# Optimization experiments

Measured on AMD Instinct MI355X. Metric: run time of the kernel, lower is better.

The kernel has to match this reference:

```python
import jax, jax.numpy as jnp
import numpy as np

B, C, H, W = 16, 256, 32, 32
NH, DH = 16, 16          # n_heads, n_head_channels; NH*DH == C
STRIDE, KK = 2, 9        # offset conv stride / kernel (stage_idx=0)
Hk, Wk = 16, 16          # offset map size = H/stride
NS = Hk * Wk             # n_sample
EPS_LN, EPS_BN = 1e-5, 1e-5


def conv1x1(x, w, b=None):
    # x: [B,Ci,H,W], w: [Co,Ci]
    y = jnp.einsum('bihw,oi->bohw', x, w)
    if b is not None:
        y = y + b[None, :, None, None]
    return y


def dwconv(x, w, b):
    # depthwise conv, w: [C,1,KK,KK]
    y = jax.lax.conv_general_dilated(
        x, w, (STRIDE, STRIDE), [(KK // 2, KK // 2)] * 2,
        dimension_numbers=('NCHW', 'OIHW', 'NCHW'),
        feature_group_count=x.shape[1])
    return y + b[None, :, None, None]


def ln_channels(x, g, b):
    # LayerNormProxy: layer-norm over channel dim of NCHW
    m = jnp.mean(x, axis=1, keepdims=True)
    v = jnp.mean((x - m) ** 2, axis=1, keepdims=True)
    return (x - m) / jnp.sqrt(v + EPS_LN) * g[None, :, None, None] + b[None, :, None, None]


def ref_points(hk, wk, b):
    # normalized (y, x) reference grid in [-1, 1], matching _get_ref_points
    ry = (jnp.arange(hk, dtype=jnp.float32) + 0.5) / hk * 2.0 - 1.0
    rx = (jnp.arange(wk, dtype=jnp.float32) + 0.5) / wk * 2.0 - 1.0
    ref = jnp.stack(jnp.meshgrid(ry, rx, indexing='ij'), axis=-1)  # [hk,wk,2] (y,x)
    return jnp.broadcast_to(ref[None], (b, hk, wk, 2))


def grid_sample_bilinear(img, grid):
    # img: [B,C,H,W]; grid: [B,Hg,Wg,2] in (x,y) order, [-1,1], align_corners=True,
    # zeros padding (matches torch F.grid_sample defaults).
    Bi, Ci, Hi, Wi = img.shape
    gx = (grid[..., 0] + 1.0) * 0.5 * (Wi - 1)
    gy = (grid[..., 1] + 1.0) * 0.5 * (Hi - 1)
    x0 = jnp.floor(gx); y0 = jnp.floor(gy)
    x1 = x0 + 1.0;      y1 = y0 + 1.0
    wx1 = gx - x0; wx0 = 1.0 - wx1
    wy1 = gy - y0; wy0 = 1.0 - wy1
    imgf = img.reshape(Bi, Ci, Hi * Wi)

    def gather(yi, xi):
        valid = (yi >= 0) & (yi < Hi) & (xi >= 0) & (xi < Wi)
        idx = (jnp.clip(yi, 0, Hi - 1) * Wi + jnp.clip(xi, 0, Wi - 1)).astype(jnp.int32)
        v = jnp.take_along_axis(imgf, idx.reshape(Bi, 1, -1), axis=2)  # [B,C,Hg*Wg]
        return v * valid.reshape(Bi, 1, -1).astype(img.dtype)

    out = (gather(y0, x0) * (wy0 * wx0).reshape(Bi, 1, -1)
           + gather(y0, x1) * (wy0 * wx1).reshape(Bi, 1, -1)
           + gather(y1, x0) * (wy1 * wx0).reshape(Bi, 1, -1)
           + gather(y1, x1) * (wy1 * wx1).reshape(Bi, 1, -1))
    return out.reshape(Bi, Ci, grid.shape[1], grid.shape[2])


def setup_inputs() -> dict:
    key = jax.random.key(0)
    ks = jax.random.split(key, 16)
    s = 0.05
    return {
        'x':        jax.random.normal(ks[0], (B, C, H, W), jnp.float32),
        'wq':       jax.random.normal(ks[1], (C, C), jnp.float32) * s,
        'bq':       jax.random.normal(ks[2], (C,), jnp.float32) * s,
        'off_dw_w': jax.random.normal(ks[3], (C, 1, KK, KK), jnp.float32) * s,
        'off_dw_b': jax.random.normal(ks[4], (C,), jnp.float32) * s,
        'ln_g':     jnp.ones((C,), jnp.float32),
        'ln_b':     jnp.zeros((C,), jnp.float32),
        'off_pw_w': jax.random.normal(ks[5], (2, C), jnp.float32) * s,
        'wk':       jax.random.normal(ks[6], (C, C), jnp.float32) * s,
        'bk':       jax.random.normal(ks[7], (C,), jnp.float32) * s,
        'wv':       jax.random.normal(ks[8], (C, C), jnp.float32) * s,
        'bv':       jax.random.normal(ks[9], (C,), jnp.float32) * s,
        'wo':       jax.random.normal(ks[10], (C, C), jnp.float32) * s,
        'bo':       jax.random.normal(ks[11], (C,), jnp.float32) * s,
        'bn_g':     jnp.ones((C,), jnp.float32),
        'bn_b':     jnp.zeros((C,), jnp.float32),
        'bn_m':     jax.random.normal(ks[12], (C,), jnp.float32) * s,
        'bn_v':     jax.random.uniform(ks[13], (C,), jnp.float32) + 0.5,
    }


def reference(x, wq, bq, off_dw_w, off_dw_b, ln_g, ln_b, off_pw_w,
              wk, bk, wv, bv, wo, bo, bn_g, bn_b, bn_m, bn_v):
    q = conv1x1(x, wq, bq)                                 # [B,C,H,W]
    # offset branch (n_groups=1 so q_off == q)
    off = dwconv(q, off_dw_w, off_dw_b)                    # [B,C,Hk,Wk]
    off = jax.nn.gelu(ln_channels(off, ln_g, ln_b), approximate=False)
    offset = jnp.einsum('bihw,oi->bohw', off, off_pw_w)    # [B,2,Hk,Wk] (y,x)
    offset = jnp.transpose(offset, (0, 2, 3, 1))           # [B,Hk,Wk,2]
    ref = ref_points(Hk, Wk, B)
    pos = jnp.tanh(offset + ref)                           # offset_range_factor[0] < 0 branch
    # deformable sampling: grid takes (x,y)
    xs = grid_sample_bilinear(x, pos[..., ::-1])           # [B,C,Hk,Wk]
    xs = xs.reshape(B, C, 1, NS)
    k = conv1x1(xs, wk, bk).reshape(B * NH, DH, NS)
    v = conv1x1(xs, wv, bv).reshape(B * NH, DH, NS)
    qf = q.reshape(B * NH, DH, H * W)
    attn = jnp.einsum('bcm,bcn->bmn', qf, k) * (DH ** -0.5)  # [B*NH, H*W, NS]
    attn = jax.nn.softmax(attn, axis=2)
    out = jnp.einsum('bmn,bcn->bcm', attn, v).reshape(B, C, H, W)
    y = conv1x1(out, wo, bo)
    # BatchNorm2d in eval mode with running stats
    y = ((y - bn_m[None, :, None, None]) / jnp.sqrt(bn_v[None, :, None, None] + EPS_BN)
         * bn_g[None, :, None, None] + bn_b[None, :, None, None])
    return y
```

## Files before the change

kernel.cpp:

```cpp
#include <hip/hip_runtime.h>
#include <hip/hip_bf16.h>
#include <math.h>

#define BATCH 16
#define CH    256
#define HW    1024
#define NS    256
#define NH    16
#define DH    16

typedef __attribute__((ext_vector_type(8))) short short8v;
typedef __attribute__((ext_vector_type(4))) float float4v;

__device__ __forceinline__ unsigned short f2bf(float f) {
    return __builtin_bit_cast(unsigned short, __float2bfloat16(f));
}
__device__ __forceinline__ unsigned pack2(float lo, float hi) {
    return (unsigned)f2bf(lo) | ((unsigned)f2bf(hi) << 16);
}

__global__ __launch_bounds__(256) void prep_k(
    const float* __restrict__ wq, const float* __restrict__ wk,
    const float* __restrict__ wv, const float* __restrict__ wo,
    unsigned short* __restrict__ Wf,
    const float* __restrict__ x, unsigned short* __restrict__ xT)
{
    int blk = blockIdx.x;
    if (blk < 1024) {
        const float* W;
        switch (blk >> 8) {
            case 0: W = wq; break;
            case 1: W = wk; break;
            case 2: W = wv; break;
            default: W = wo; break;
        }
        int e = (blk & 255) * 256 + threadIdx.x;
        int i = e & 7, l = (e >> 3) & 63, kt = (e >> 9) & 7, ot = e >> 12;
        float v = W[(ot * 16 + (l & 15)) * 256 + kt * 32 + 8 * (l >> 4) + i];
        Wf[(blk >> 8) * 65536 + e] = f2bf(v);
    } else {
        int xb = blk - 1024;
        int b = xb >> 4, pblk = (xb >> 2) & 3, cblk = xb & 3;
        int p = pblk * 256 + threadIdx.x;
        const float* xp = x + (size_t)b * CH * HW + p;
        unsigned short* o = xT + ((size_t)b * HW + p) * CH;
        #pragma unroll
        for (int cc = 0; cc < 64; cc += 8) {
            int c0 = cblk * 64 + cc;
            short8v t;
            #pragma unroll
            for (int i = 0; i < 8; ++i) t[i] = (short)f2bf(xp[(size_t)(c0 + i) * HW]);
            *(short8v*)&o[c0] = t;
        }
    }
}

template<int P, int MODE>
__global__ __launch_bounds__(256) void gemm_k(
    const unsigned short* __restrict__ Wf, const unsigned short* __restrict__ XT,
    const float* __restrict__ bias,
    float* __restrict__ outF, unsigned short* __restrict__ outB,
    const float* __restrict__ bn_g, const float* __restrict__ bn_b,
    const float* __restrict__ bn_m, const float* __restrict__ bn_v)
{
    const int b = blockIdx.z;

    const int t = threadIdx.x, lane = t & 63, wvi = t >> 6;
    const int g = lane >> 4, col = lane & 15;
    const int o0 = blockIdx.x * 64;
    const int p0 = blockIdx.y * 128 + wvi * 32;
    const unsigned short* xb = XT + ((size_t)b * P + p0) * CH;

    float4v acc[4][2];
    #pragma unroll
    for (int mi = 0; mi < 4; ++mi)
        #pragma unroll
        for (int ni = 0; ni < 2; ++ni) {
            float4v z = {0.f, 0.f, 0.f, 0.f};
            acc[mi][ni] = z;
        }

    #pragma unroll
    for (int kt = 0; kt < 8; ++kt) {
        short8v af[4], bf[2];
        #pragma unroll
        for (int mi = 0; mi < 4; ++mi)
            af[mi] = *(const short8v*)&Wf[(((((o0 >> 4) + mi) * 8) + kt) * 64 + lane) * 8];
        #pragma unroll
        for (int ni = 0; ni < 2; ++ni) {
            if (MODE == 2) {
                const int hh = kt * 2 + (g >> 1);
                const int p  = p0 + ni * 16 + col;
                bf[ni] = *(const short8v*)&XT[(((size_t)(b * 16 + hh) * P + p) << 4) + 8 * (g & 1)];
            } else {
                bf[ni] = *(const short8v*)&xb[(size_t)(ni * 16 + col) * CH + kt * 32 + 8 * g];
            }
        }
        #pragma unroll
        for (int mi = 0; mi < 4; ++mi)
            #pragma unroll
            for (int ni = 0; ni < 2; ++ni)
                acc[mi][ni] = __builtin_amdgcn_mfma_f32_16x16x32_bf16(
                    af[mi], bf[ni], acc[mi][ni], 0, 0, 0);
    }

    #pragma unroll
    for (int mi = 0; mi < 4; ++mi) {
        const int ob = o0 + mi * 16 + 4 * g;
        float bs[4];
        #pragma unroll
        for (int ii = 0; ii < 4; ++ii) bs[ii] = bias[ob + ii];

        if (MODE == 2) {
            float sc[4], sh[4];
            #pragma unroll
            for (int ii = 0; ii < 4; ++ii) {
                int o = ob + ii;
                float s = bn_g[o] * rsqrtf(bn_v[o] + 1e-5f);
                sc[ii] = s;
                sh[ii] = bn_b[o] - bn_m[o] * s + bs[ii] * s;
            }
            #pragma unroll
            for (int ni = 0; ni < 2; ++ni) {
                int p = p0 + ni * 16 + col;
                #pragma unroll
                for (int ii = 0; ii < 4; ++ii)
                    outF[((size_t)(b * CH + ob + ii)) * P + p] =
                        acc[mi][ni][ii] * sc[ii] + sh[ii];
            }
        } else {
            const int hh = (o0 >> 4) + mi;
            #pragma unroll
            for (int ni = 0; ni < 2; ++ni) {
                int p = p0 + ni * 16 + col;
                float v0 = acc[mi][ni][0] + bs[0];
                float v1 = acc[mi][ni][1] + bs[1];
                float v2 = acc[mi][ni][2] + bs[2];
                float v3 = acc[mi][ni][3] + bs[3];
                outF[((size_t)(b * CH + ob + 0)) * P + p] = v0;
                outF[((size_t)(b * CH + ob + 1)) * P + p] = v1;
                outF[((size_t)(b * CH + ob + 2)) * P + p] = v2;
                outF[((size_t)(b * CH + ob + 3)) * P + p] = v3;
                uint2 w;
                w.x = pack2(v0 * 0.25f, v1 * 0.25f);
                w.y = pack2(v2 * 0.25f, v3 * 0.25f);
                *(uint2*)&outB[(((size_t)(b * 16 + hh) * P + p) << 4) + 4 * g] = w;
            }
        }
    }
}

__global__ __launch_bounds__(256) void dwconv_k(
    const float* __restrict__ q, const float* __restrict__ w,
    const float* __restrict__ bias, float* __restrict__ off)
{
    int bc = blockIdx.x;
    int c  = bc & (CH - 1);
    __shared__ float plane[HW];
    __shared__ float kw[81];
    int t = threadIdx.x;
    const float* qp = q + (size_t)bc * HW;
    #pragma unroll
    for (int j = t; j < HW; j += 256) plane[j] = qp[j];
    if (t < 81) kw[t] = w[c * 81 + t];
    __syncthreads();
    int hk = t >> 4, wk = t & 15;
    float s = bias[c];
    int yb = hk * 2 - 4, xb = wk * 2 - 4;
    #pragma unroll
    for (int dy = 0; dy < 9; ++dy) {
        int yy = yb + dy;
        if ((unsigned)yy < 32u) {
            #pragma unroll
            for (int dx = 0; dx < 9; ++dx) {
                int xx = xb + dx;
                if ((unsigned)xx < 32u) s += kw[dy * 9 + dx] * plane[yy * 32 + xx];
            }
        }
    }
    off[(size_t)bc * NS + t] = s;
}

__device__ inline void block_reduce2(float& a, float& b, int t, float* sbuf)
{
    #pragma unroll
    for (int o = 32; o > 0; o >>= 1) {
        a += __shfl_down(a, o);
        b += __shfl_down(b, o);
    }
    int w = t >> 6;
    if ((t & 63) == 0) { sbuf[w * 2] = a; sbuf[w * 2 + 1] = b; }
    __syncthreads();
    a = sbuf[0] + sbuf[2] + sbuf[4] + sbuf[6];
    b = sbuf[1] + sbuf[3] + sbuf[5] + sbuf[7];
    __syncthreads();
}

__global__ __launch_bounds__(256) void lngs_k(
    const float* __restrict__ off, const float* __restrict__ ln_g,
    const float* __restrict__ ln_b, const float* __restrict__ pw,
    const float* __restrict__ x, unsigned short* __restrict__ xsT)
{
    __shared__ float sbuf[8];
    int bs = blockIdx.x;
    int b = bs >> 8, s = bs & 255;
    int c = threadIdx.x;
    float v = off[((size_t)(b * CH + c)) * NS + s];
    float a = v, q2 = v * v;
    block_reduce2(a, q2, c, sbuf);
    float mean = a * (1.0f / 256.0f);
    float var  = q2 * (1.0f / 256.0f) - mean * mean;
    float xn = (v - mean) * rsqrtf(var + 1e-5f) * ln_g[c] + ln_b[c];
    float g = 0.5f * xn * (1.0f + erff(xn * 0.70710678118654752f));
    float d0 = g * pw[c];
    float d1 = g * pw[CH + c];
    block_reduce2(d0, d1, c, sbuf);

    int hk = s >> 4, wk = s & 15;
    float ry = ((hk + 0.5f) / 16.0f) * 2.0f - 1.0f;
    float rx = ((wk + 0.5f) / 16.0f) * 2.0f - 1.0f;
    float py = tanhf(d0 + ry);
    float px = tanhf(d1 + rx);

    float gx = (px + 1.0f) * 0.5f * 31.0f;
    float gy = (py + 1.0f) * 0.5f * 31.0f;
    float x0f = floorf(gx), y0f = floorf(gy);
    int ix = (int)x0f, iy = (int)y0f;
    float wx1 = gx - x0f, wx0 = 1.0f - wx1;
    float wy1 = gy - y0f, wy0 = 1.0f - wy1;
    const float* img = x + ((size_t)b * CH + c) * HW;
    float v00 = ((unsigned)iy < 32u && (unsigned)ix < 32u) ? img[iy * 32 + ix] : 0.0f;
    float v01 = ((unsigned)iy < 32u && (unsigned)(ix + 1) < 32u) ? img[iy * 32 + ix + 1] : 0.0f;
    float v10 = ((unsigned)(iy + 1) < 32u && (unsigned)ix < 32u) ? img[(iy + 1) * 32 + ix] : 0.0f;
    float v11 = ((unsigned)(iy + 1) < 32u && (unsigned)(ix + 1) < 32u) ? img[(iy + 1) * 32 + ix + 1] : 0.0f;
    float vv = wy0 * wx0 * v00 + wy0 * wx1 * v01 + wy1 * wx0 * v10 + wy1 * wx1 * v11;
    xsT[(size_t)bs * CH + c] = f2bf(vv);
}

__global__ __launch_bounds__(1024) void attn_fused_k(
    const unsigned short* __restrict__ qH, const unsigned short* __restrict__ xsT,
    const unsigned short* __restrict__ Wf,
    const float* __restrict__ bk, const float* __restrict__ bv,
    unsigned short* __restrict__ aoH)
{
    const int bh    = blockIdx.x >> 1;
    const int mhalf = blockIdx.x & 1;
    const int b = bh >> 4, h = bh & 15;

    __shared__ short Kp[16 * 32 * 8 + 8];
    __shared__ short Vp[8 * 64 * 8];
    __shared__ short Ps[16][16 * 32];

    const int tid  = threadIdx.x;
    const int lane = tid & 63;
    const int wvi  = tid >> 6;
    const int col  = lane & 15;
    const int g    = lane >> 4;

    {
        const unsigned short* WfK = Wf + 1 * 65536 + h * 4096;
        const unsigned short* WfV = Wf + 2 * 65536 + h * 4096;
        float bk4[4];
        #pragma unroll
        for (int j = 0; j < 4; ++j) bk4[j] = bk[h * 16 + 4 * g + j];
        const float bvv = bv[h * 16 + col];

        const int t  = wvi;
        const int n0 = t * 16;
        float4v accK = {0.f, 0.f, 0.f, 0.f};
        float4v accV = {0.f, 0.f, 0.f, 0.f};
        #pragma unroll
        for (int kt = 0; kt < 8; ++kt) {
            short8v xsf = *(const short8v*)&xsT[((size_t)(b * NS + n0 + col)) * CH + kt * 32 + 8 * g];
            short8v wkf = *(const short8v*)&WfK[(kt * 64 + lane) * 8];
            short8v wvf = *(const short8v*)&WfV[(kt * 64 + lane) * 8];
            accK = __builtin_amdgcn_mfma_f32_16x16x32_bf16(wkf, xsf, accK, 0, 0, 0);
            accV = __builtin_amdgcn_mfma_f32_16x16x32_bf16(xsf, wvf, accV, 0, 0, 0);
        }
        uint2 wrk;
        wrk.x = pack2(accK[0] + bk4[0], accK[1] + bk4[1]);
        wrk.y = pack2(accK[2] + bk4[2], accK[3] + bk4[3]);
        *(uint2*)&Kp[(t * 32 + (g >> 1) * 16 + col) * 8 + 4 * (g & 1)] = wrk;
        uint2 wrv;
        wrv.x = pack2(accV[0] + bvv, accV[1] + bvv);
        wrv.y = pack2(accV[2] + bvv, accV[3] + bvv);
        *(uint2*)&Vp[((t >> 1) * 64 + col + 16 * ((2 * t + (g >> 1)) & 3)) * 8 + 4 * (g & 1)] = wrv;
    }
    if (tid == 0) {
        short8v z = {0, 0, 0, 0, 0, 0, 0, 0};
        *(short8v*)&Kp[16 * 32 * 8] = z;
    }
    __syncthreads();

    const unsigned short* Qb = qH + ((size_t)(b * 16 + h) * HW << 4);
    unsigned short*       Ob = aoH + ((size_t)(b * 16 + h) * HW << 4);
    char* pbase = (char*)Ps[wvi];
    const char* kbase = (const char*)Kp + ((lane < 32) ? lane * 16 : 16 * 32 * 16);
    const int   kstep = (lane < 32) ? 512 : 0;

    #pragma unroll
    for (int mt = 0; mt < 2; ++mt) {
        const int m0 = mhalf * 512 + wvi * 32 + mt * 16;

        short8v qf = {0, 0, 0, 0, 0, 0, 0, 0};
        if (g < 2)
            qf = *(const short8v*)&Qb[((m0 + col) << 4) + 8 * g];

        float4v p[16];
        #pragma unroll
        for (int t = 0; t < 16; ++t) {
            short8v kf = *(const short8v*)(kbase + t * kstep);
            float4v z = {0.f, 0.f, 0.f, 0.f};
            p[t] = __builtin_amdgcn_mfma_f32_16x16x32_bf16(kf, qf, z, 0, 0, 0);
        }

        float mx4[16];
        #pragma unroll
        for (int t = 0; t < 16; ++t)
            mx4[t] = fmaxf(fmaxf(p[t][0], p[t][1]), fmaxf(p[t][2], p[t][3]));
        #pragma unroll
        for (int o = 8; o >= 1; o >>= 1)
            #pragma unroll
            for (int i = 0; i < 8; ++i)
                if (i < o) mx4[i] = fmaxf(mx4[i], mx4[i + o]);
        float mx = mx4[0];
        mx = fmaxf(mx, __shfl_xor(mx, 16));
        mx = fmaxf(mx, __shfl_xor(mx, 32));

        float s4[4] = {0.f, 0.f, 0.f, 0.f};
        #pragma unroll
        for (int t = 0; t < 16; ++t) {
            #pragma unroll
            for (int i = 0; i < 4; ++i) {
                float e = __expf(p[t][i] - mx);
                p[t][i] = e;
                s4[i] += e;
            }
        }
        float sum = (s4[0] + s4[1]) + (s4[2] + s4[3]);
        sum += __shfl_xor(sum, 16);
        sum += __shfl_xor(sum, 32);
        const float inv = 1.0f / sum;

        float4v acc = {0.f, 0.f, 0.f, 0.f};
        #pragma unroll
        for (int c = 0; c < 8; ++c) {
            #pragma unroll
            for (int pp = 0; pp < 2; ++pp) {
                float4v pv = p[2 * c + pp];
                uint2 wr;
                wr.x = pack2(pv[0], pv[1]);
                wr.y = pack2(pv[2], pv[3]);
                *(uint2*)(pbase + ((col * 64 + (16 * pp + 4 * g) * 2) ^ ((col & 7) << 4))) = wr;
            }
            short8v pf = *(const short8v*)(pbase + ((col * 64 + 16 * g) ^ ((col & 7) << 4)));
            short8v vf = *(const short8v*)&Vp[(c * 64 + lane) * 8];
            acc = __builtin_amdgcn_mfma_f32_16x16x32_bf16(vf, pf, acc, 0, 0, 0);
        }

        uint2 w;
        w.x = pack2(acc[0] * inv, acc[1] * inv);
        w.y = pack2(acc[2] * inv, acc[3] * inv);
        *(uint2*)&Ob[((m0 + col) << 4) + 4 * g] = w;
    }
}

extern "C" void kernel_launch(void* const* d_in, const int* in_sizes, int n_in,
                              void* d_out, int out_size, void* d_ws, size_t ws_size,
                              hipStream_t stream)
{
    const float* x        = (const float*)d_in[0];
    const float* wq       = (const float*)d_in[1];
    const float* bq       = (const float*)d_in[2];
    const float* off_dw_w = (const float*)d_in[3];
    const float* off_dw_b = (const float*)d_in[4];
    const float* ln_g     = (const float*)d_in[5];
    const float* ln_b     = (const float*)d_in[6];
    const float* off_pw_w = (const float*)d_in[7];
    const float* wk       = (const float*)d_in[8];
    const float* bk       = (const float*)d_in[9];
    const float* wv       = (const float*)d_in[10];
    const float* bv       = (const float*)d_in[11];
    const float* wo       = (const float*)d_in[12];
    const float* bo       = (const float*)d_in[13];
    const float* bn_g     = (const float*)d_in[14];
    const float* bn_b     = (const float*)d_in[15];
    const float* bn_m     = (const float*)d_in[16];
    const float* bn_v     = (const float*)d_in[17];

    float* ws  = (float*)d_ws;
    float* q   = ws;
    float* off = q + 4194304;
    unsigned short* us  = (unsigned short*)(off + 1048576);
    unsigned short* Wf  = us;
    unsigned short* xT  = Wf  + 262144;
    unsigned short* qH  = xT  + 4194304;
    unsigned short* xsT = qH  + 4194304;
    unsigned short* aoH = xsT + 1048576;

    prep_k<<<1280, 256, 0, stream>>>(wq, wk, wv, wo, Wf, x, xT);
    gemm_k<HW, 0><<<dim3(4, 8, BATCH), 256, 0, stream>>>(
        Wf, xT, bq, q, qH, nullptr, nullptr, nullptr, nullptr);
    dwconv_k<<<BATCH * CH, 256, 0, stream>>>(q, off_dw_w, off_dw_b, off);
    lngs_k<<<BATCH * NS, 256, 0, stream>>>(off, ln_g, ln_b, off_pw_w, x, xsT);
    attn_fused_k<<<BATCH * NH * 2, 1024, 0, stream>>>(qH, xsT, Wf, bk, bv, aoH);
    gemm_k<HW, 2><<<dim3(4, 8, BATCH), 256, 0, stream>>>(
        Wf + 3 * 65536, aoH, bo, (float*)d_out, nullptr,
        bn_g, bn_b, bn_m, bn_v);
}
```

Before: 110.6 us.

## Fuse x transpose and bf16 conversion into Q projection GEMM via LDS staging

The separate prep kernel is removed. The Q-projection GEMM now loads fp32 x directly, converts it to bf16 and stages it in swizzled shared memory, and converts wq on the fly; the same launch also packs the k/v/o weights. This drops a kernel launch and the round trip of the transposed bf16 xT buffer through global memory. In exchange, x is read once per output-channel tile, and the kernel adds barriers and per-iteration fp32 weight conversion. Separately, bounds checks in the bilinear gather are dropped because tanh keeps sample coordinates inside the image.

Result: slower. 115.3 us (+4.3%).

```diff
diff --git a/kernel.cpp b/kernel.cpp
--- a/kernel.cpp
+++ b/kernel.cpp
@@ -18,58 +18,137 @@
 __device__ __forceinline__ unsigned pack2(float lo, float hi) {
     return (unsigned)f2bf(lo) | ((unsigned)f2bf(hi) << 16);
 }
-
-__global__ __launch_bounds__(256) void prep_k(
+__device__ __forceinline__ short8v pack8(float4 a, float4 b) {
+    short8v r;
+    r[0] = (short)f2bf(a.x); r[1] = (short)f2bf(a.y);
+    r[2] = (short)f2bf(a.z); r[3] = (short)f2bf(a.w);
+    r[4] = (short)f2bf(b.x); r[5] = (short)f2bf(b.y);
+    r[6] = (short)f2bf(b.z); r[7] = (short)f2bf(b.w);
+    return r;
+}
+
+__global__ __launch_bounds__(256) void gemmq_k(
     const float* __restrict__ wq, const float* __restrict__ wk,
     const float* __restrict__ wv, const float* __restrict__ wo,
-    unsigned short* __restrict__ Wf,
-    const float* __restrict__ x, unsigned short* __restrict__ xT)
-{
-    int blk = blockIdx.x;
-    if (blk < 1024) {
-        const float* W;
-        switch (blk >> 8) {
-            case 0: W = wq; break;
-            case 1: W = wk; break;
-            case 2: W = wv; break;
-            default: W = wo; break;
-        }
-        int e = (blk & 255) * 256 + threadIdx.x;
-        int i = e & 7, l = (e >> 3) & 63, kt = (e >> 9) & 7, ot = e >> 12;
-        float v = W[(ot * 16 + (l & 15)) * 256 + kt * 32 + 8 * (l >> 4) + i];
-        Wf[(blk >> 8) * 65536 + e] = f2bf(v);
-    } else {
-        int xb = blk - 1024;
-        int b = xb >> 4, pblk = (xb >> 2) & 3, cblk = xb & 3;
-        int p = pblk * 256 + threadIdx.x;
-        const float* xp = x + (size_t)b * CH * HW + p;
-        unsigned short* o = xT + ((size_t)b * HW + p) * CH;
-        #pragma unroll
-        for (int cc = 0; cc < 64; cc += 8) {
-            int c0 = cblk * 64 + cc;
-            short8v t;
-            #pragma unroll
-            for (int i = 0; i < 8; ++i) t[i] = (short)f2bf(xp[(size_t)(c0 + i) * HW]);
-            *(short8v*)&o[c0] = t;
-        }
-    }
-}
-
-template<int P, int MODE>
-__global__ __launch_bounds__(256) void gemm_k(
+    const float* __restrict__ x, const float* __restrict__ bias,
+    float* __restrict__ q, unsigned short* __restrict__ qH,
+    unsigned short* __restrict__ Wf)
+{
+    const int blk = blockIdx.x;
+    if (blk >= 512) {
+        int e = (blk - 512) * 256 + threadIdx.x;
+        int mat = e >> 16;
+        int ee = e & 65535;
+        const float* W = (mat == 0) ? wk : (mat == 1) ? wv : wo;
+        int i = ee & 7, l = (ee >> 3) & 63, kt = (ee >> 9) & 7, ot = ee >> 12;
+        Wf[(mat + 1) * 65536 + ee] =
+            f2bf(W[(ot * 16 + (l & 15)) * 256 + kt * 32 + 8 * (l >> 4) + i]);
+        return;
+    }
+
+    const int b  = blk & 15;
+    const int py = (blk >> 4) & 7;
+    const int ox = blk >> 7;
+
+    __shared__ short Bs[128 * 32];
+
+    const int t = threadIdx.x, lane = t & 63, wvi = t >> 6;
+    const int g = lane >> 4, col = lane & 15;
+    const int o0 = ox * 64;
+    const int p0 = py * 128;
+    const int pw = wvi * 32;
+    const float* xb = x + (size_t)b * CH * HW;
+
+    const int oct = t >> 6;
+    const int pl  = t & 63;
+
+    float4v acc[4][2];
+    #pragma unroll
+    for (int mi = 0; mi < 4; ++mi)
+        #pragma unroll
+        for (int ni = 0; ni < 2; ++ni) {
+            float4v z = {0.f, 0.f, 0.f, 0.f};
+            acc[mi][ni] = z;
+        }
+
+    char* bsb = (char*)Bs;
+
+    for (int kt = 0; kt < 8; ++kt) {
+        #pragma unroll
+        for (int pass = 0; pass < 2; ++pass) {
+            const int p = pass * 64 + pl;
+            const int c0 = oct * 8;
+            float4 lo, hi;
+            lo.x = xb[(size_t)(kt * 32 + c0 + 0) * HW + p0 + p];
+            lo.y = xb[(size_t)(kt * 32 + c0 + 1) * HW + p0 + p];
+            lo.z = xb[(size_t)(kt * 32 + c0 + 2) * HW + p0 + p];
+            lo.w = xb[(size_t)(kt * 32 + c0 + 3) * HW + p0 + p];
+            hi.x = xb[(size_t)(kt * 32 + c0 + 4) * HW + p0 + p];
+            hi.y = xb[(size_t)(kt * 32 + c0 + 5) * HW + p0 + p];
+            hi.z = xb[(size_t)(kt * 32 + c0 + 6) * HW + p0 + p];
+            hi.w = xb[(size_t)(kt * 32 + c0 + 7) * HW + p0 + p];
+            short8v v = pack8(lo, hi);
+            *(short8v*)(bsb + ((p * 64 + c0 * 2) ^ ((p & 7) << 4))) = v;
+        }
+        __syncthreads();
+
+        short8v af[4], bf[2];
+        #pragma unroll
+        for (int mi = 0; mi < 4; ++mi) {
+            const float* wp = wq + (size_t)(o0 + mi * 16 + col) * CH + kt * 32 + 8 * g;
+            af[mi] = pack8(*(const float4*)wp, *(const float4*)(wp + 4));
+        }
+        #pragma unroll
+        for (int ni = 0; ni < 2; ++ni) {
+            const int p = pw + ni * 16 + col;
+            bf[ni] = *(const short8v*)(bsb + ((p * 64 + 16 * g) ^ ((p & 7) << 4)));
+        }
+        #pragma unroll
+        for (int mi = 0; mi < 4; ++mi)
+            #pragma unroll
+            for (int ni = 0; ni < 2; ++ni)
+                acc[mi][ni] = __builtin_amdgcn_mfma_f32_16x16x32_bf16(
+                    af[mi], bf[ni], acc[mi][ni], 0, 0, 0);
+        __syncthreads();
+    }
+
+    #pragma unroll
+    for (int mi = 0; mi < 4; ++mi) {
+        const int ob = o0 + mi * 16 + 4 * g;
+        const int hh = (o0 >> 4) + mi;
+        float bs[4];
+        #pragma unroll
+        for (int ii = 0; ii < 4; ++ii) bs[ii] = bias[ob + ii];
+        #pragma unroll
+        for (int ni = 0; ni < 2; ++ni) {
+            int p = p0 + pw + ni * 16 + col;
+            float v0 = acc[mi][ni][0] + bs[0];
+            float v1 = acc[mi][ni][1] + bs[1];
+            float v2 = acc[mi][ni][2] + bs[2];
+            float v3 = acc[mi][ni][3] + bs[3];
+            q[((size_t)(b * CH + ob + 0)) * HW + p] = v0;
+            q[((size_t)(b * CH + ob + 1)) * HW + p] = v1;
+            q[((size_t)(b * CH + ob + 2)) * HW + p] = v2;
+            q[((size_t)(b * CH + ob + 3)) * HW + p] = v3;
+            uint2 w;
+            w.x = pack2(v0 * 0.25f, v1 * 0.25f);
+            w.y = pack2(v2 * 0.25f, v3 * 0.25f);
+            *(uint2*)&qH[(((size_t)(b * 16 + hh) * HW + p) << 4) + 4 * g] = w;
+        }
+    }
+}
+
+__global__ __launch_bounds__(256) void gemmo_k(
     const unsigned short* __restrict__ Wf, const unsigned short* __restrict__ XT,
-    const float* __restrict__ bias,
-    float* __restrict__ outF, unsigned short* __restrict__ outB,
+    const float* __restrict__ bias, float* __restrict__ outF,
     const float* __restrict__ bn_g, const float* __restrict__ bn_b,
     const float* __restrict__ bn_m, const float* __restrict__ bn_v)
 {
     const int b = blockIdx.z;
-
     const int t = threadIdx.x, lane = t & 63, wvi = t >> 6;
     const int g = lane >> 4, col = lane & 15;
     const int o0 = blockIdx.x * 64;
     const int p0 = blockIdx.y * 128 + wvi * 32;
-    const unsigned short* xb = XT + ((size_t)b * P + p0) * CH;
 
     float4v acc[4][2];
     #pragma unroll
@@ -88,13 +167,9 @@
             af[mi] = *(const short8v*)&Wf[(((((o0 >> 4) + mi) * 8) + kt) * 64 + lane) * 8];
         #pragma unroll
         for (int ni = 0; ni < 2; ++ni) {
-            if (MODE == 2) {
-                const int hh = kt * 2 + (g >> 1);
-                const int p  = p0 + ni * 16 + col;
-                bf[ni] = *(const short8v*)&XT[(((size_t)(b * 16 + hh) * P + p) << 4) + 8 * (g & 1)];
-            } else {
-                bf[ni] = *(const short8v*)&xb[(size_t)(ni * 16 + col) * CH + kt * 32 + 8 * g];
-            }
+            const int hh = kt * 2 + (g >> 1);
+            const int p  = p0 + ni * 16 + col;
+            bf[ni] = *(const short8v*)&XT[(((size_t)(b * 16 + hh) * HW + p) << 4) + 8 * (g & 1)];
         }
         #pragma unroll
         for (int mi = 0; mi < 4; ++mi)
@@ -107,45 +182,21 @@
     #pragma unroll
     for (int mi = 0; mi < 4; ++mi) {
         const int ob = o0 + mi * 16 + 4 * g;
-        float bs[4];
-        #pragma unroll
-        for (int ii = 0; ii < 4; ++ii) bs[ii] = bias[ob + ii];
-
-        if (MODE == 2) {
-            float sc[4], sh[4];
-            #pragma unroll
-            for (int ii = 0; ii < 4; ++ii) {
-                int o = ob + ii;
-                float s = bn_g[o] * rsqrtf(bn_v[o] + 1e-5f);
-                sc[ii] = s;
-                sh[ii] = bn_b[o] - bn_m[o] * s + bs[ii] * s;
-            }
-            #pragma unroll
-            for (int ni = 0; ni < 2; ++ni) {
-                int p = p0 + ni * 16 + col;
-                #pragma unroll
-                for (int ii = 0; ii < 4; ++ii)
-                    outF[((size_t)(b * CH + ob + ii)) * P + p] =
-                        acc[mi][ni][ii] * sc[ii] + sh[ii];
-            }
-        } else {
-            const int hh = (o0 >> 4) + mi;
-            #pragma unroll
-            for (int ni = 0; ni < 2; ++ni) {
-                int p = p0 + ni * 16 + col;
-                float v0 = acc[mi][ni][0] + bs[0];
-                float v1 = acc[mi][ni][1] + bs[1];
-                float v2 = acc[mi][ni][2] + bs[2];
-                float v3 = acc[mi][ni][3] + bs[3];
-                outF[((size_t)(b * CH + ob + 0)) * P + p] = v0;
-                outF[((size_t)(b * CH + ob + 1)) * P + p] = v1;
-                outF[((size_t)(b * CH + ob + 2)) * P + p] = v2;
-                outF[((size_t)(b * CH + ob + 3)) * P + p] = v3;
-                uint2 w;
-                w.x = pack2(v0 * 0.25f, v1 * 0.25f);
-                w.y = pack2(v2 * 0.25f, v3 * 0.25f);
-                *(uint2*)&outB[(((size_t)(b * 16 + hh) * P + p) << 4) + 4 * g] = w;
-            }
+        float sc[4], sh[4];
+        #pragma unroll
+        for (int ii = 0; ii < 4; ++ii) {
+            int o = ob + ii;
+            float s = bn_g[o] * rsqrtf(bn_v[o] + 1e-5f);
+            sc[ii] = s;
+            sh[ii] = bn_b[o] - bn_m[o] * s + bias[o] * s;
+        }
+        #pragma unroll
+        for (int ni = 0; ni < 2; ++ni) {
+            int p = p0 + ni * 16 + col;
+            #pragma unroll
+            for (int ii = 0; ii < 4; ++ii)
+                outF[((size_t)(b * CH + ob + ii)) * HW + p] =
+                    acc[mi][ni][ii] * sc[ii] + sh[ii];
         }
     }
 }
@@ -229,10 +280,10 @@
     float wx1 = gx - x0f, wx0 = 1.0f - wx1;
     float wy1 = gy - y0f, wy0 = 1.0f - wy1;
     const float* img = x + ((size_t)b * CH + c) * HW;
-    float v00 = ((unsigned)iy < 32u && (unsigned)ix < 32u) ? img[iy * 32 + ix] : 0.0f;
-    float v01 = ((unsigned)iy < 32u && (unsigned)(ix + 1) < 32u) ? img[iy * 32 + ix + 1] : 0.0f;
-    float v10 = ((unsigned)(iy + 1) < 32u && (unsigned)ix < 32u) ? img[(iy + 1) * 32 + ix] : 0.0f;
-    float v11 = ((unsigned)(iy + 1) < 32u && (unsigned)(ix + 1) < 32u) ? img[(iy + 1) * 32 + ix + 1] : 0.0f;
+    float v00 = img[iy * 32 + ix];
+    float v01 = img[iy * 32 + ix + 1];
+    float v10 = img[(iy + 1) * 32 + ix];
+    float v11 = img[(iy + 1) * 32 + ix + 1];
     float vv = wy0 * wx0 * v00 + wy0 * wx1 * v01 + wy1 * wx0 * v10 + wy1 * wx1 * v11;
     xsT[(size_t)bs * CH + c] = f2bf(vv);
 }
@@ -393,18 +444,14 @@
     float* off = q + 4194304;
     unsigned short* us  = (unsigned short*)(off + 1048576);
     unsigned short* Wf  = us;
-    unsigned short* xT  = Wf  + 262144;
-    unsigned short* qH  = xT  + 4194304;
+    unsigned short* qH  = Wf  + 262144;
     unsigned short* xsT = qH  + 4194304;
     unsigned short* aoH = xsT + 1048576;
 
-    prep_k<<<1280, 256, 0, stream>>>(wq, wk, wv, wo, Wf, x, xT);
-    gemm_k<HW, 0><<<dim3(4, 8, BATCH), 256, 0, stream>>>(
-        Wf, xT, bq, q, qH, nullptr, nullptr, nullptr, nullptr);
+    gemmq_k<<<1280, 256, 0, stream>>>(wq, wk, wv, wo, x, bq, q, qH, Wf);
     dwconv_k<<<BATCH * CH, 256, 0, stream>>>(q, off_dw_w, off_dw_b, off);
     lngs_k<<<BATCH * NS, 256, 0, stream>>>(off, ln_g, ln_b, off_pw_w, x, xsT);
     attn_fused_k<<<BATCH * NH * 2, 1024, 0, stream>>>(qH, xsT, Wf, bk, bv, aoH);
-    gemm_k<HW, 2><<<dim3(4, 8, BATCH), 256, 0, stream>>>(
-        Wf + 3 * 65536, aoH, bo, (float*)d_out, nullptr,
-        bn_g, bn_b, bn_m, bn_v);
-}
+    gemmo_k<<<dim3(4, 8, BATCH), 256, 0, stream>>>(
+        Wf + 3 * 65536, aoH, bo, (float*)d_out, bn_g, bn_b, bn_m, bn_v);
+}
```
